# Optimization experiments

Hardware: AMD Instinct MI355X
Metric: run time of the kernel (lower is better)

## Reference

```python
import jax, jax.numpy as jnp
import numpy as np

N_HEADS = 16
N_QUBITS = 7
DIM = 2 ** N_QUBITS  # per-head state dimension = 128


def _rotation_gates(params):
    """params: [H, nq, 3] -> composite Rz@Ry@Rx gates [H, nq, 2, 2] complex64."""
    a = params[..., 0] / 2.0
    b = params[..., 1] / 2.0
    c = params[..., 2] / 2.0
    ca, sa = jnp.cos(a), jnp.sin(a)
    cb, sb = jnp.cos(b), jnp.sin(b)
    i_ = jnp.complex64(1j)
    rx = jnp.stack([jnp.stack([ca + 0j, -i_ * sa], -1),
                    jnp.stack([-i_ * sa, ca + 0j], -1)], -2)  # [H,nq,2,2]
    ry = jnp.stack([jnp.stack([cb + 0j, -sb + 0j], -1),
                    jnp.stack([sb + 0j, cb + 0j], -1)], -2)
    z = jnp.zeros_like(c) + 0j
    rz = jnp.stack([jnp.stack([jnp.exp(-i_ * c), z], -1),
                    jnp.stack([z, jnp.exp(i_ * c)], -1)], -2)
    return jnp.einsum('...ij,...jk,...kl->...il', rz, ry, rx).astype(jnp.complex64)


def _quantum_transform(states, params):
    """states: [B,S,H,D] real; params: [H,nq,3]. Apply per-qubit gates then measure |psi|^2.
    Qubit q acts on axis q of the state reshaped to [2]*n_qubits (q=0 most significant)."""
    B, S, H, D = states.shape
    gates = _rotation_gates(params)  # [H, nq, 2, 2]
    psi = states.astype(jnp.complex64)
    for q in range(N_QUBITS):
        L = 2 ** q
        R = D // (2 * L)
        psi = psi.reshape(B, S, H, L, 2, R)
        psi = jnp.einsum('hij,bshljr->bshlir', gates[:, q], psi)
        psi = psi.reshape(B, S, H, D)
    return psi.real ** 2 + psi.imag ** 2  # measurement probabilities, real fp32


def setup_inputs() -> dict:
    key = jax.random.key(0)
    ks = jax.random.split(key, 6)
    B, S = 2, 2048
    return {
        'states': jax.random.normal(ks[0], (B, S, N_HEADS * DIM), dtype=jnp.float32),
        'attention_mask': jnp.ones((B, S), dtype=jnp.int32),
        'query_params': jax.random.normal(ks[1], (N_HEADS, N_QUBITS, 3), dtype=jnp.float32),
        'key_params': jax.random.normal(ks[2], (N_HEADS, N_QUBITS, 3), dtype=jnp.float32),
        'value_params': jax.random.normal(ks[3], (N_HEADS, N_QUBITS, 3), dtype=jnp.float32),
        'W_out': jax.random.normal(ks[4], (DIM, N_HEADS * DIM), dtype=jnp.float32) / np.sqrt(N_HEADS * DIM),
        'b_out': jnp.zeros((DIM,), dtype=jnp.float32),
    }


def reference(states, attention_mask, query_params, key_params, value_params, W_out, b_out):
    B, S, F = states.shape
    x = states.reshape(B, S, N_HEADS, DIM)  # split heads
    q = _quantum_transform(x, query_params)   # [B,S,H,D]
    k = _quantum_transform(x, key_params)
    v = _quantum_transform(x, value_params)
    scores = jnp.einsum('bqhd,bkhd->bhqk', q, k) / np.sqrt(DIM)  # [B,H,S,S]
    mask = attention_mask[:, None, None, :] != 0  # [B,1,1,S]
    scores = jnp.where(mask, scores, jnp.float32(-jnp.inf))
    probs = jax.nn.softmax(scores, axis=-1)
    ctx = jnp.einsum('bhqk,bkhd->bqhd', probs, v)  # [B,S,H,D]
    concat = ctx.reshape(B, S, N_HEADS * DIM)
    return concat @ W_out.T + b_out  # [B,S,D]
```

## Files before the change

### kernel.cpp

```cpp
#include <hip/hip_runtime.h>
#include <math.h>

#define NH 16
#define DD 128
#define SS 2048
#define NQ 7

typedef __attribute__((ext_vector_type(8))) short bf16x8;
typedef __attribute__((ext_vector_type(16))) float f32x16;

#define MFMA32(a,b,c) __builtin_amdgcn_mfma_f32_32x32x16_bf16(a,b,c,0,0,0)

__device__ __forceinline__ unsigned pkbf(float a, float b){
    unsigned ua = __float_as_uint(a); ua += 0x7FFF + ((ua>>16)&1);
    unsigned ub = __float_as_uint(b); ub += 0x7FFF + ((ub>>16)&1);
    return (ua>>16) | (ub & 0xFFFF0000u);
}

__device__ __forceinline__ float fexp2(float x){
#if __has_builtin(__builtin_amdgcn_exp2f)
    return __builtin_amdgcn_exp2f(x);
#else
    return __expf(x * 0.69314718056f);
#endif
}

__device__ __forceinline__ void gl_lds16(const int4* g, int4* l){
    __builtin_amdgcn_global_load_lds((const __attribute__((address_space(1))) void*)g,
                                     (__attribute__((address_space(3))) void*)l, 16, 0, 0);
}

struct cplx { float r, i; };
__device__ __forceinline__ cplx cmul(cplx a, cplx b){ cplx o; o.r = a.r*b.r - a.i*b.i; o.i = a.r*b.i + a.i*b.r; return o; }
__device__ __forceinline__ cplx cadd(cplx a, cplx b){ cplx o; o.r = a.r+b.r; o.i = a.i+b.i; return o; }

__global__ void gates_kernel(const float* __restrict__ qp, const float* __restrict__ kp,
                             const float* __restrict__ vp, float* __restrict__ gates){
    for (int it = threadIdx.x; it < 3*NH*NQ; it += 256){
        int set = it / (NH*NQ);
        int rem = it % (NH*NQ);
        const float* p = (set==0 ? qp : (set==1 ? kp : vp)) + rem*3;
        float a = p[0]*0.5f, b = p[1]*0.5f, c = p[2]*0.5f;
        float ca=cosf(a), sa=sinf(a), cb=cosf(b), sb=sinf(b), cc=cosf(c), sc=sinf(c);
        cplx rx00={ca,0.f}, rx01={0.f,-sa}, rx10={0.f,-sa}, rx11={ca,0.f};
        cplx ry00={cb,0.f}, ry01={-sb,0.f}, ry10={sb,0.f}, ry11={cb,0.f};
        cplx e0={cc,-sc}, e1={cc,sc};
        cplx m00 = cadd(cmul(ry00,rx00), cmul(ry01,rx10));
        cplx m01 = cadd(cmul(ry00,rx01), cmul(ry01,rx11));
        cplx m10 = cadd(cmul(ry10,rx00), cmul(ry11,rx10));
        cplx m11 = cadd(cmul(ry10,rx01), cmul(ry11,rx11));
        cplx g00 = cmul(e0,m00), g01 = cmul(e0,m01), g10 = cmul(e1,m10), g11 = cmul(e1,m11);
        float* gp = gates + it*8;
        gp[0]=g00.r; gp[1]=g00.i; gp[2]=g01.r; gp[3]=g01.i;
        gp[4]=g10.r; gp[5]=g10.i; gp[6]=g11.r; gp[7]=g11.i;
    }
}

__global__ __launch_bounds__(256) void prep2_kernel(const float* __restrict__ W,
        const float* __restrict__ gates, ushort* __restrict__ wfrag, ushort* __restrict__ ufrag){
    int t = threadIdx.x;
    if (blockIdx.x < 128){
        int tid = blockIdx.x*256 + t;
        int ln = tid & 31, hi = (tid>>5)&1, ds = (tid>>6)&127, ct = tid>>13;
        int n = ct*32 + ln;
        const float* src = W + (size_t)n*2048 + ds*16 + hi*8;
        float4 f0 = *(const float4*)(src);
        float4 f1 = *(const float4*)(src + 4);
        int4 o;
        o.x = (int)pkbf(f0.x, f0.y); o.y = (int)pkbf(f0.z, f0.w);
        o.z = (int)pkbf(f1.x, f1.y); o.w = (int)pkbf(f1.z, f1.w);
        ((int4*)wfrag)[tid] = o;
        return;
    }
    int sh = blockIdx.x - 128;
    const float* gp = gates + sh*NQ*8;
    float g[7][8];
    #pragma unroll
    for (int q=0;q<7;++q)
        #pragma unroll
        for (int e=0;e<8;++e) g[q][e] = gp[q*8+e];
    int4* uf = (int4*)ufrag;
    #pragma unroll
    for (int p=0;p<8;++p){
        int pos = t + p*256;
        int ln = pos & 31, hi = (pos>>5)&1, ds = (pos>>6)&7, ct = pos>>9;
        int dp = ct*32 + ln;
        int d0 = ds*16 + hi*8;
        cplx base = {1.f, 0.f};
        #pragma unroll
        for (int q=0;q<4;++q){
            int rb = (dp >> (6-q)) & 1, cb2 = (d0 >> (6-q)) & 1;
            cplx gv = { g[q][rb*4+cb2*2], g[q][rb*4+cb2*2+1] };
            base = cmul(base, gv);
        }
        int r4 = (dp>>2)&1, r5 = (dp>>1)&1, r6 = dp&1;
        float vr[8], vi[8];
        #pragma unroll
        for (int j=0;j<8;++j){
            cplx g4 = { g[4][r4*4 + ((j>>2)&1)*2], g[4][r4*4 + ((j>>2)&1)*2 + 1] };
            cplx g5 = { g[5][r5*4 + ((j>>1)&1)*2], g[5][r5*4 + ((j>>1)&1)*2 + 1] };
            cplx g6 = { g[6][r6*4 + (j&1)*2],      g[6][r6*4 + (j&1)*2 + 1] };
            cplx v = cmul(cmul(cmul(base, g4), g5), g6);
            vr[j] = v.r; vi[j] = v.i;
        }
        int4 outr, outi;
        outr.x = (int)pkbf(vr[0],vr[1]); outr.y = (int)pkbf(vr[2],vr[3]);
        outr.z = (int)pkbf(vr[4],vr[5]); outr.w = (int)pkbf(vr[6],vr[7]);
        outi.x = (int)pkbf(vi[0],vi[1]); outi.y = (int)pkbf(vi[2],vi[3]);
        outi.z = (int)pkbf(vi[4],vi[5]); outi.w = (int)pkbf(vi[6],vi[7]);
        uf[ ((sh*8 + ct)*8 + ds)*64 + hi*32 + ln ]     = outr;
        uf[ ((sh*8 + 4 + ct)*8 + ds)*64 + hi*32 + ln ] = outi;
    }
}

__global__ __launch_bounds__(256) void qkv_kernel(const float* __restrict__ states,
        const ushort* __restrict__ ufrag, ushort* __restrict__ qfo,
        ushort* __restrict__ kfo, ushort* __restrict__ vfo){
    __shared__ int xs[128*66];
    int t = threadIdx.x, w = t>>6, lane = t&63, hi = lane>>5, ln = lane&31;
    int blk = blockIdx.x;
    int set = blk >> 9;
    int r9  = blk & 511;
    int bh = r9 >> 4, stile = r9 & 15;
    int b = bh >> 4, h = bh & 15;
    const float sc = 0.12751743f;
    {
        int c = t & 31, tk2 = t >> 5;
        #pragma unroll
        for (int i=0;i<16;++i){
            int tk = i*8 + tk2;
            const float* src = states + ((size_t)(b*SS + stile*128 + tk))*2048 + h*128 + c*4;
            float4 f = *(const float4*)src;
            int2 o; o.x = (int)pkbf(f.x,f.y); o.y = (int)pkbf(f.z,f.w);
            *(int2*)(xs + tk*66 + c*2) = o;
        }
    }
    __syncthreads();
    int ct = w;
    int sh = set*16 + h;
    const int4* ub = (const int4*)ufrag;
    int4* qf4 = (int4*)qfo; int4* kf4 = (int4*)kfo; int4* vf4 = (int4*)vfo;
    bf16x8 ur[8], ui[8];
    #pragma unroll
    for (int ds=0; ds<8; ++ds){
        ur[ds] = *(const bf16x8*)(ub + ((sh*8 + ct)*8 + ds)*64 + lane);
        ui[ds] = *(const bf16x8*)(ub + ((sh*8 + 4 + ct)*8 + ds)*64 + lane);
    }
    #pragma unroll 1
    for (int tt=0; tt<4; ++tt){
        bf16x8 xf[8];
        #pragma unroll
        for (int ds=0; ds<8; ++ds){
            union { bf16x8 v; int2 d[2]; } c;
            const int2* base = (const int2*)(xs + (tt*32 + ln)*66 + ds*8 + hi*4);
            c.d[0] = base[0]; c.d[1] = base[1];
            xf[ds] = c.v;
        }
        f32x16 Cr, Ci;
        #pragma unroll
        for (int r=0;r<16;++r){ Cr[r]=0.f; Ci[r]=0.f; }
        if (set < 2){
            #pragma unroll
            for (int ds=0; ds<8; ++ds){
                Cr = MFMA32(ur[ds], xf[ds], Cr);
                Ci = MFMA32(ui[ds], xf[ds], Ci);
            }
        } else {
            #pragma unroll
            for (int ds=0; ds<8; ++ds){
                Cr = MFMA32(xf[ds], ur[ds], Cr);
                Ci = MFMA32(xf[ds], ui[ds], Ci);
            }
        }
        float pv[16];
        #pragma unroll
        for (int r=0;r<16;++r) pv[r] = Cr[r]*Cr[r] + Ci[r]*Ci[r];
        if (set == 0){
            #pragma unroll
            for (int r=0;r<16;++r) pv[r] *= sc;
        }
        unsigned u2[4][2];
        #pragma unroll
        for (int g2=0; g2<4; ++g2){
            u2[g2][0] = pkbf(pv[g2*4+0], pv[g2*4+1]);
            u2[g2][1] = pkbf(pv[g2*4+2], pv[g2*4+3]);
        }
        int mt = stile*4 + tt;
        #pragma unroll
        for (int gg=0; gg<2; ++gg){
            int g2s = hi*2 + gg, g2p = g2s ^ 2;
            unsigned r0 = (unsigned)__shfl_xor((int)u2[g2p][0], 32);
            unsigned r1 = (unsigned)__shfl_xor((int)u2[g2p][1], 32);
            int4 frag;
            frag.x = (int)(hi ? r0 : u2[g2s][0]);
            frag.y = (int)(hi ? r1 : u2[g2s][1]);
            frag.z = (int)(hi ? u2[g2s][0] : r0);
            frag.w = (int)(hi ? u2[g2s][1] : r1);
            if (set == 0)
                qf4[((bh*64 + mt)*8 + ct*2 + hi)*64 + gg*32 + ln] = frag;
            else if (set == 1)
                kf4[((bh*64 + mt)*8 + ct*2 + hi)*64 + gg*32 + ln] = frag;
            else
                vf4[((bh*4 + ct)*128 + mt*2 + hi)*64 + gg*32 + ln] = frag;
        }
    }
}

__global__ __launch_bounds__(256, 3) void flash_kernel(const ushort* __restrict__ qfi,
        const ushort* __restrict__ kfi, const ushort* __restrict__ vfi,
        const int* __restrict__ mask, ushort* __restrict__ ctxf){
    __shared__ __align__(16) int4 kbuf[2][512];
    __shared__ __align__(16) int4 vbuf[2][512];
    int t = threadIdx.x, w = t>>6, lane = t&63, hi = lane>>5, ln = lane&31;
    int bid = blockIdx.x;
    int i2 = bid >> 3;
    int bh = (bid & 7)*4 + (i2 & 3);
    int qt = i2 >> 2;
    int b = bh >> 4;
    const float NEGC = -57.7078018f;
    const int4* qfp = (const int4*)qfi + (size_t)((bh*64 + qt*4 + w)*8)*64 + lane;
    bf16x8 qf[8];
    #pragma unroll
    for (int ds=0; ds<8; ++ds) qf[ds] = *(const bf16x8*)(qfp + ds*64);
    const int4* kroot = (const int4*)kfi + (size_t)(bh*64)*8*64 + lane;
    const int4* vroot = (const int4*)vfi + (size_t)(bh*4)*128*64 + lane;
    const int* mp = mask + b*SS;
    f32x16 O[4];
    #pragma unroll
    for (int d=0; d<4; ++d){
        #pragma unroll
        for (int r=0;r<16;++r) O[d][r] = 0.f;
    }
    float l0=0.f, l1=0.f, l2=0.f, l3=0.f;
    auto stage = [&](int kt, int pb){
        if (w < 2){
            int dsb = w*4;
            const int4* src = kroot + ((size_t)kt*8 + dsb)*64;
            int4* dst = &kbuf[pb][dsb*64];
            #pragma unroll
            for (int j=0;j<4;++j) gl_lds16(src + j*64, dst + j*64);
        } else {
            #pragma unroll
            for (int j=0;j<4;++j){
                int v = (w-2)*4 + j;
                int db = v>>1, tt = v&1;
                const int4* src = vroot + ((size_t)db*128 + kt*2 + tt)*64;
                gl_lds16(src, &vbuf[pb][v*64]);
            }
        }
    };
    stage(0, 0);
    for (int kt=0; kt<64; ++kt){
        int p = kt & 1;
        int mk = mp[kt*32 + ln];
        __syncthreads();
        if (kt < 63) stage(kt+1, p^1);
        const int4* kl = kbuf[p];
        const int4* vl = vbuf[p];
        f32x16 S;
        #pragma unroll
        for (int r=0;r<16;++r) S[r] = NEGC;
        #pragma unroll
        for (int ds=0; ds<8; ++ds){
            bf16x8 kk = *(const bf16x8*)(kl + ds*64 + lane);
            S = MFMA32(kk, qf[ds], S);
        }
        if (__ballot(mk != 0) != ~0ull){
            #pragma unroll
            for (int r=0;r<16;++r){
                int row0 = ((r>>2)<<3) + (hi<<2) + (r&3);
                if (__shfl(mk, row0) == 0) S[r] = -1e30f;
            }
        }
        #pragma unroll
        for (int r=0;r<16;++r) S[r] = fexp2(S[r]);
        #pragma unroll
        for (int r=0;r<16;r+=4){
            l0 += S[r]; l1 += S[r+1]; l2 += S[r+2]; l3 += S[r+3];
        }
        #pragma unroll
        for (int T=0; T<2; ++T){
            unsigned A0 = pkbf(S[8*T+0], S[8*T+1]);
            unsigned A1 = pkbf(S[8*T+2], S[8*T+3]);
            unsigned B0 = pkbf(S[8*T+4], S[8*T+5]);
            unsigned B1 = pkbf(S[8*T+6], S[8*T+7]);
            unsigned X0 = hi ? A0 : B0, X1 = hi ? A1 : B1;
            unsigned Y0 = (unsigned)__shfl_xor((int)X0, 32);
            unsigned Y1 = (unsigned)__shfl_xor((int)X1, 32);
            union { bf16x8 v; unsigned u[4]; } pf;
            pf.u[0] = hi ? Y0 : A0;
            pf.u[1] = hi ? Y1 : A1;
            pf.u[2] = hi ? B0 : Y0;
            pf.u[3] = hi ? B1 : Y1;
            #pragma unroll
            for (int db=0; db<4; ++db){
                bf16x8 vf = *(const bf16x8*)(vl + (db*2 + T)*64 + lane);
                O[db] = MFMA32(vf, pf.v, O[db]);
            }
        }
    }
    float l = (l0+l1) + (l2+l3);
    l += __shfl_xor(l, 32);
    float inv = 1.f / l;
    int h = bh & 15;
    int mt = b*64 + qt*4 + w;
    int4* cf = (int4*)ctxf;
    #pragma unroll
    for (int db=0; db<4; ++db){
        unsigned u[4][2];
        #pragma unroll
        for (int g2=0; g2<4; ++g2){
            u[g2][0] = pkbf(O[db][g2*4+0]*inv, O[db][g2*4+1]*inv);
            u[g2][1] = pkbf(O[db][g2*4+2]*inv, O[db][g2*4+3]*inv);
        }
        #pragma unroll
        for (int gg=0; gg<2; ++gg){
            int g2s = hi*2 + gg;
            int g2p = g2s ^ 2;
            unsigned r0 = (unsigned)__shfl_xor((int)u[g2p][0], 32);
            unsigned r1 = (unsigned)__shfl_xor((int)u[g2p][1], 32);
            int4 frag;
            frag.x = (int)(hi ? r0 : u[g2s][0]);
            frag.y = (int)(hi ? r1 : u[g2s][1]);
            frag.z = (int)(hi ? u[g2s][0] : r0);
            frag.w = (int)(hi ? u[g2s][1] : r1);
            int ds = h*8 + db*2 + hi;
            cf[ ((size_t)(mt*128 + ds)*2 + gg)*32 + ln ] = frag;
        }
    }
}

__global__ __launch_bounds__(256) void proj_kernel(const ushort* __restrict__ ctxf,
                                                   const ushort* __restrict__ wfrag,
                                                   const float* __restrict__ bo,
                                                   float* __restrict__ out){
    int t = threadIdx.x, w = t >> 6, lane = t & 63;
    int hi = lane >> 5, ln = lane & 31;
    int mt = blockIdx.x, ct = w;
    const int4* A = (const int4*)ctxf + (size_t)mt*8192 + lane;
    const int4* B = (const int4*)wfrag + (size_t)ct*8192 + lane;
    f32x16 acc;
    #pragma unroll
    for (int r=0;r<16;++r) acc[r] = 0.f;
    #pragma unroll 8
    for (int ds=0; ds<128; ++ds){
        bf16x8 a = *(const bf16x8*)(A + (size_t)ds*64);
        bf16x8 b = *(const bf16x8*)(B + (size_t)ds*64);
        acc = MFMA32(a, b, acc);
    }
    float bias = bo[ct*32 + ln];
    float* op = out + (size_t)(mt*32)*128 + ct*32 + ln;
    #pragma unroll
    for (int r=0;r<16;++r){
        int row = (r&3) + 8*(r>>2) + 4*hi;
        op[(size_t)row*128] = acc[r] + bias;
    }
}

extern "C" void kernel_launch(void* const* d_in, const int* in_sizes, int n_in,
                              void* d_out, int out_size, void* d_ws, size_t ws_size,
                              hipStream_t stream){
    const float* states = (const float*)d_in[0];
    const int*   mask   = (const int*)d_in[1];
    const float* qp     = (const float*)d_in[2];
    const float* kp     = (const float*)d_in[3];
    const float* vp     = (const float*)d_in[4];
    const float* W      = (const float*)d_in[5];
    const float* bo     = (const float*)d_in[6];
    float* out = (float*)d_out;
    char* wsb = (char*)d_ws;
    float*  gates = (float*) wsb;
    ushort* wfrag = (ushort*)(wsb + 16384);
    ushort* ufrag = (ushort*)(wsb + 16384 + 524288);
    char*   big   = wsb + 16384 + 524288 + 3145728;
    ushort* qf    = (ushort*)(big);
    ushort* kf    = (ushort*)(big + 1u*16777216);
    ushort* vf    = (ushort*)(big + 2u*16777216);
    ushort* ctxf  = (ushort*)(big + 3u*16777216);
    hipLaunchKernelGGL(gates_kernel, dim3(1), dim3(256), 0, stream, qp, kp, vp, gates);
    hipLaunchKernelGGL(prep2_kernel, dim3(176), dim3(256), 0, stream, W, gates, wfrag, ufrag);
    hipLaunchKernelGGL(qkv_kernel, dim3(1536), dim3(256), 0, stream, states, ufrag, qf, kf, vf);
    hipLaunchKernelGGL(flash_kernel, dim3(512), dim3(256), 0, stream, qf, kf, vf, mask, ctxf);
    hipLaunchKernelGGL(proj_kernel, dim3(128), dim3(256), 0, stream, ctxf, wfrag, bo, out);
}
```

Baseline: 263.7 us.

## Fuse gate computation into prep, split QKV tiles, and split-K the projection

```diff
diff --git a/kernel.cpp b/kernel.cpp
--- a/kernel.cpp
+++ b/kernel.cpp
@@ -34,30 +34,9 @@
 __device__ __forceinline__ cplx cmul(cplx a, cplx b){ cplx o; o.r = a.r*b.r - a.i*b.i; o.i = a.r*b.i + a.i*b.r; return o; }
 __device__ __forceinline__ cplx cadd(cplx a, cplx b){ cplx o; o.r = a.r+b.r; o.i = a.i+b.i; return o; }
 
-__global__ void gates_kernel(const float* __restrict__ qp, const float* __restrict__ kp,
-                             const float* __restrict__ vp, float* __restrict__ gates){
-    for (int it = threadIdx.x; it < 3*NH*NQ; it += 256){
-        int set = it / (NH*NQ);
-        int rem = it % (NH*NQ);
-        const float* p = (set==0 ? qp : (set==1 ? kp : vp)) + rem*3;
-        float a = p[0]*0.5f, b = p[1]*0.5f, c = p[2]*0.5f;
-        float ca=cosf(a), sa=sinf(a), cb=cosf(b), sb=sinf(b), cc=cosf(c), sc=sinf(c);
-        cplx rx00={ca,0.f}, rx01={0.f,-sa}, rx10={0.f,-sa}, rx11={ca,0.f};
-        cplx ry00={cb,0.f}, ry01={-sb,0.f}, ry10={sb,0.f}, ry11={cb,0.f};
-        cplx e0={cc,-sc}, e1={cc,sc};
-        cplx m00 = cadd(cmul(ry00,rx00), cmul(ry01,rx10));
-        cplx m01 = cadd(cmul(ry00,rx01), cmul(ry01,rx11));
-        cplx m10 = cadd(cmul(ry10,rx00), cmul(ry11,rx10));
-        cplx m11 = cadd(cmul(ry10,rx01), cmul(ry11,rx11));
-        cplx g00 = cmul(e0,m00), g01 = cmul(e0,m01), g10 = cmul(e1,m10), g11 = cmul(e1,m11);
-        float* gp = gates + it*8;
-        gp[0]=g00.r; gp[1]=g00.i; gp[2]=g01.r; gp[3]=g01.i;
-        gp[4]=g10.r; gp[5]=g10.i; gp[6]=g11.r; gp[7]=g11.i;
-    }
-}
-
-__global__ __launch_bounds__(256) void prep2_kernel(const float* __restrict__ W,
-        const float* __restrict__ gates, ushort* __restrict__ wfrag, ushort* __restrict__ ufrag){
+__global__ __launch_bounds__(256) void prep2_kernel(const float* __restrict__ qp,
+        const float* __restrict__ kp, const float* __restrict__ vp,
+        const float* __restrict__ W, ushort* __restrict__ wfrag, ushort* __restrict__ ufrag){
     int t = threadIdx.x;
     if (blockIdx.x < 128){
         int tid = blockIdx.x*256 + t;
@@ -73,12 +52,29 @@
         return;
     }
     int sh = blockIdx.x - 128;
-    const float* gp = gates + sh*NQ*8;
+    __shared__ float gs[7][8];
+    if (t < 7){
+        int set = sh >> 4, h = sh & 15;
+        const float* p = (set==0 ? qp : (set==1 ? kp : vp)) + (h*NQ + t)*3;
+        float a = p[0]*0.5f, b = p[1]*0.5f, c = p[2]*0.5f;
+        float ca=cosf(a), sa=sinf(a), cb=cosf(b), sb=sinf(b), cc=cosf(c), sc=sinf(c);
+        cplx rx00={ca,0.f}, rx01={0.f,-sa}, rx10={0.f,-sa}, rx11={ca,0.f};
+        cplx ry00={cb,0.f}, ry01={-sb,0.f}, ry10={sb,0.f}, ry11={cb,0.f};
+        cplx e0={cc,-sc}, e1={cc,sc};
+        cplx m00 = cadd(cmul(ry00,rx00), cmul(ry01,rx10));
+        cplx m01 = cadd(cmul(ry00,rx01), cmul(ry01,rx11));
+        cplx m10 = cadd(cmul(ry10,rx00), cmul(ry11,rx10));
+        cplx m11 = cadd(cmul(ry10,rx01), cmul(ry11,rx11));
+        cplx g00 = cmul(e0,m00), g01 = cmul(e0,m01), g10 = cmul(e1,m10), g11 = cmul(e1,m11);
+        gs[t][0]=g00.r; gs[t][1]=g00.i; gs[t][2]=g01.r; gs[t][3]=g01.i;
+        gs[t][4]=g10.r; gs[t][5]=g10.i; gs[t][6]=g11.r; gs[t][7]=g11.i;
+    }
+    __syncthreads();
     float g[7][8];
     #pragma unroll
     for (int q=0;q<7;++q)
         #pragma unroll
-        for (int e=0;e<8;++e) g[q][e] = gp[q*8+e];
+        for (int e=0;e<8;++e) g[q][e] = gs[q][e];
     int4* uf = (int4*)ufrag;
     #pragma unroll
     for (int p=0;p<8;++p){
@@ -113,23 +109,23 @@
     }
 }
 
-__global__ __launch_bounds__(256) void qkv_kernel(const float* __restrict__ states,
+__global__ __launch_bounds__(256, 2) void qkv_kernel(const float* __restrict__ states,
         const ushort* __restrict__ ufrag, ushort* __restrict__ qfo,
         ushort* __restrict__ kfo, ushort* __restrict__ vfo){
-    __shared__ int xs[128*66];
+    __shared__ int xs[64*66];
     int t = threadIdx.x, w = t>>6, lane = t&63, hi = lane>>5, ln = lane&31;
     int blk = blockIdx.x;
-    int set = blk >> 9;
-    int r9  = blk & 511;
-    int bh = r9 >> 4, stile = r9 & 15;
+    int set = blk >> 10;
+    int r10 = blk & 1023;
+    int bh = r10 >> 5, stile = r10 & 31;
     int b = bh >> 4, h = bh & 15;
     const float sc = 0.12751743f;
     {
         int c = t & 31, tk2 = t >> 5;
         #pragma unroll
-        for (int i=0;i<16;++i){
+        for (int i=0;i<8;++i){
             int tk = i*8 + tk2;
-            const float* src = states + ((size_t)(b*SS + stile*128 + tk))*2048 + h*128 + c*4;
+            const float* src = states + ((size_t)(b*SS + stile*64 + tk))*2048 + h*128 + c*4;
             float4 f = *(const float4*)src;
             int2 o; o.x = (int)pkbf(f.x,f.y); o.y = (int)pkbf(f.z,f.w);
             *(int2*)(xs + tk*66 + c*2) = o;
@@ -147,7 +143,7 @@
         ui[ds] = *(const bf16x8*)(ub + ((sh*8 + 4 + ct)*8 + ds)*64 + lane);
     }
     #pragma unroll 1
-    for (int tt=0; tt<4; ++tt){
+    for (int tt=0; tt<2; ++tt){
         bf16x8 xf[8];
         #pragma unroll
         for (int ds=0; ds<8; ++ds){
@@ -185,7 +181,7 @@
             u2[g2][0] = pkbf(pv[g2*4+0], pv[g2*4+1]);
             u2[g2][1] = pkbf(pv[g2*4+2], pv[g2*4+3]);
         }
-        int mt = stile*4 + tt;
+        int mt = stile*2 + tt;
         #pragma unroll
         for (int gg=0; gg<2; ++gg){
             int g2s = hi*2 + gg, g2p = g2s ^ 2;
@@ -206,7 +202,7 @@
     }
 }
 
-__global__ __launch_bounds__(256, 3) void flash_kernel(const ushort* __restrict__ qfi,
+__global__ __launch_bounds__(256, 2) void flash_kernel(const ushort* __restrict__ qfi,
         const ushort* __restrict__ kfi, const ushort* __restrict__ vfi,
         const int* __restrict__ mask, ushort* __restrict__ ctxf){
     __shared__ __align__(16) int4 kbuf[2][512];
@@ -334,26 +330,35 @@
                                                    const ushort* __restrict__ wfrag,
                                                    const float* __restrict__ bo,
                                                    float* __restrict__ out){
+    __shared__ float ls[3][16][64];
     int t = threadIdx.x, w = t >> 6, lane = t & 63;
     int hi = lane >> 5, ln = lane & 31;
-    int mt = blockIdx.x, ct = w;
-    const int4* A = (const int4*)ctxf + (size_t)mt*8192 + lane;
-    const int4* B = (const int4*)wfrag + (size_t)ct*8192 + lane;
+    int mt = blockIdx.x >> 2, ct = blockIdx.x & 3;
+    const int4* A = (const int4*)ctxf + (size_t)mt*8192 + (size_t)w*32*64 + lane;
+    const int4* B = (const int4*)wfrag + (size_t)ct*8192 + (size_t)w*32*64 + lane;
     f32x16 acc;
     #pragma unroll
     for (int r=0;r<16;++r) acc[r] = 0.f;
     #pragma unroll 8
-    for (int ds=0; ds<128; ++ds){
+    for (int ds=0; ds<32; ++ds){
         bf16x8 a = *(const bf16x8*)(A + (size_t)ds*64);
         bf16x8 b = *(const bf16x8*)(B + (size_t)ds*64);
         acc = MFMA32(a, b, acc);
     }
-    float bias = bo[ct*32 + ln];
-    float* op = out + (size_t)(mt*32)*128 + ct*32 + ln;
-    #pragma unroll
-    for (int r=0;r<16;++r){
-        int row = (r&3) + 8*(r>>2) + 4*hi;
-        op[(size_t)row*128] = acc[r] + bias;
+    if (w > 0){
+        #pragma unroll
+        for (int r=0;r<16;++r) ls[w-1][r][lane] = acc[r];
+    }
+    __syncthreads();
+    if (w == 0){
+        float bias = bo[ct*32 + ln];
+        float* op = out + (size_t)(mt*32)*128 + ct*32 + ln;
+        #pragma unroll
+        for (int r=0;r<16;++r){
+            int row = (r&3) + 8*(r>>2) + 4*hi;
+            float s = acc[r] + ls[0][r][lane] + ls[1][r][lane] + ls[2][r][lane] + bias;
+            op[(size_t)row*128] = s;
+        }
     }
 }
 
@@ -369,7 +374,6 @@
     const float* bo     = (const float*)d_in[6];
     float* out = (float*)d_out;
     char* wsb = (char*)d_ws;
-    float*  gates = (float*) wsb;
     ushort* wfrag = (ushort*)(wsb + 16384);
     ushort* ufrag = (ushort*)(wsb + 16384 + 524288);
     char*   big   = wsb + 16384 + 524288 + 3145728;
@@ -377,9 +381,8 @@
     ushort* kf    = (ushort*)(big + 1u*16777216);
     ushort* vf    = (ushort*)(big + 2u*16777216);
     ushort* ctxf  = (ushort*)(big + 3u*16777216);
-    hipLaunchKernelGGL(gates_kernel, dim3(1), dim3(256), 0, stream, qp, kp, vp, gates);
-    hipLaunchKernelGGL(prep2_kernel, dim3(176), dim3(256), 0, stream, W, gates, wfrag, ufrag);
-    hipLaunchKernelGGL(qkv_kernel, dim3(1536), dim3(256), 0, stream, states, ufrag, qf, kf, vf);
+    hipLaunchKernelGGL(prep2_kernel, dim3(176), dim3(256), 0, stream, qp, kp, vp, W, wfrag, ufrag);
+    hipLaunchKernelGGL(qkv_kernel, dim3(3072), dim3(256), 0, stream, states, ufrag, qf, kf, vf);
     hipLaunchKernelGGL(flash_kernel, dim3(512), dim3(256), 0, stream, qf, kf, vf, mask, ctxf);
-    hipLaunchKernelGGL(proj_kernel, dim3(128), dim3(256), 0, stream, ctxf, wfrag, bo, out);
-}
+    hipLaunchKernelGGL(proj_kernel, dim3(512), dim3(256), 0, stream, ctxf, wfrag, bo, out);
+}
```

Result: faster. 218.2 us (-17.2%).
